# Kernel tuning notes

Measured on AMD Instinct MI355X. Metric: run time of the kernel, lower is better.

The kernel has to match this reference:

```python
import jax, jax.numpy as jnp
import numpy as np
from jax import lax

B, S, D, F = 2, 4096, 1024, 4096
LN_EPS = 1e-6

def _layer_norm(x, scale, bias):
    mu = jnp.mean(x, axis=-1, keepdims=True)
    var = jnp.mean(jnp.square(x - mu), axis=-1, keepdims=True)
    return (x - mu) * lax.rsqrt(var + LN_EPS) * scale + bias

def _gate_loop(q, k, v, a):
    # max-headed GateLoop: one head per channel, scalar complex state per channel
    # h_t = a_t * h_{t-1} + k_t * v_t ; y_t = q_t * h_t
    kv = (k * v).astype(jnp.complex64)
    def comb(e1, e2):
        a1, x1 = e1
        a2, x2 = e2
        return (a1 * a2, a2 * x1 + x2)
    _, h = lax.associative_scan(comb, (a, kv), axis=1)
    return q.astype(jnp.complex64) * h

def setup_inputs() -> dict:
    key = jax.random.key(0)
    ks = jax.random.split(key, 12)
    sd = 1.0 / np.sqrt(D)
    sf = 1.0 / np.sqrt(F)
    return {
        "x": jax.random.normal(ks[0], (B, S, D), jnp.float32),
        "Wq": jax.random.normal(ks[1], (D, D), jnp.float32) * sd,
        "Wk": jax.random.normal(ks[2], (D, D), jnp.float32) * sd,
        "Wv": jax.random.normal(ks[3], (D, D), jnp.float32) * sd,
        "Wa": jax.random.normal(ks[4], (D, 2 * D), jnp.float32) * sd,
        "Wg": jax.random.normal(ks[5], (D, D), jnp.float32) * sd,
        "Wo": jax.random.normal(ks[6], (D, D), jnp.float32) * sd,
        "ln1_scale": jnp.ones((D,), jnp.float32),
        "ln1_bias": jnp.zeros((D,), jnp.float32),
        "W1": jax.random.normal(ks[7], (D, F), jnp.float32) * sd,
        "b1": jax.random.normal(ks[8], (F,), jnp.float32) * 1e-6,
        "W2": jax.random.normal(ks[9], (F, D), jnp.float32) * sf,
        "b2": jax.random.normal(ks[10], (D,), jnp.float32) * 1e-6,
        "ln2_scale": jnp.ones((D,), jnp.float32),
        "ln2_bias": jnp.zeros((D,), jnp.float32),
    }

def reference(x, Wq, Wk, Wv, Wa, Wg, Wo, ln1_scale, ln1_bias, W1, b1, W2, b2, ln2_scale, ln2_bias):
    q = x @ Wq
    k = x @ Wk
    v = x @ Wv
    a = x @ Wa
    a_real, a_imag = jnp.split(a, 2, axis=-1)
    a_c = a_real + 1j * a_imag
    magnitude = jnp.abs(a_c)
    phase = jnp.angle(a_c)
    a_c = jax.nn.sigmoid(magnitude).astype(jnp.complex64) * jnp.exp(1j * phase)
    g = x.astype(jnp.complex64) @ Wg.astype(jnp.complex64)
    y = _gate_loop(q, k, v, a_c)
    y = y * (g * jax.nn.sigmoid(g))  # silu on complex g
    y = y @ Wo.astype(jnp.complex64)
    y = y.real
    # dropout deterministic (training=False)
    y = _layer_norm(y + x, ln1_scale, ln1_bias)
    h = jax.nn.gelu(y @ W1 + b1)
    out = h @ W2 + b2
    out = _layer_norm(out + y, ln2_scale, ln2_bias)
    return out
```

## Files before the change

### kernel.cpp

```cpp
#include <hip/hip_runtime.h>
#include <cstdint>

typedef unsigned short u16;
typedef unsigned int u32;

#define AS1 __attribute__((address_space(1)))
#define AS3 __attribute__((address_space(3)))

typedef _Float16 f16x8 __attribute__((ext_vector_type(8)));
typedef float f32x4 __attribute__((ext_vector_type(4)));

static constexpr int Bb = 2, Ss = 4096, Dd = 1024, Ff = 4096;
static constexpr int Mtok = Bb * Ss;
static constexpr int NCH = 128;
static constexpr int TCH = Ss / NCH;
static constexpr int PW = 6144;

__device__ __forceinline__ float h2f(u16 u) {
    union { u16 u; _Float16 h; } w; w.u = u; return (float)w.h;
}
__device__ __forceinline__ u16 f2h(float f) {
    union { _Float16 h; u16 u; } w; w.h = (_Float16)f; return w.u;
}

__device__ __forceinline__ void gload_lds16(const u16* g, u16* l) {
    __builtin_amdgcn_global_load_lds((const AS1 u32*)g, (AS3 u32*)l, 16, 0, 0);
}

__global__ __launch_bounds__(256) void cvt_f32_f16(const float* __restrict__ src,
                                                   u16* __restrict__ dst) {
    const long i = ((long)blockIdx.x * 256 + threadIdx.x) * 4;
    float4 f = *(const float4*)(src + i);
    ushort4 o;
    o.x = f2h(f.x); o.y = f2h(f.y); o.z = f2h(f.z); o.w = f2h(f.w);
    *(ushort4*)(dst + i) = o;
}

__global__ __launch_bounds__(1024) void transpose_f32_f16(const float* __restrict__ src,
                                                          u16* __restrict__ dst,
                                                          int K, int N) {
    __shared__ u16 t[32][33];
    const int tx = threadIdx.x, ty = threadIdx.y;
    const int n0 = blockIdx.x * 32, k0 = blockIdx.y * 32;
    t[ty][tx] = f2h(src[(long)(k0 + ty) * N + n0 + tx]);
    __syncthreads();
    dst[(long)(n0 + ty) * K + k0 + tx] = t[tx][ty];
}

template <int EPI>
__global__ __launch_bounds__(256, 2) void gemm_bt(const u16* __restrict__ A,
                                                  const u16* __restrict__ BT,
                                                  u16* __restrict__ C,
                                                  const float* __restrict__ bias,
                                                  int M, int N, int K,
                                                  int lda, int ldc) {
    __shared__ __align__(16) u16 sA[128 * 32];
    __shared__ __align__(16) u16 sB[128 * 32];
    const int tid = threadIdx.x;
    const int tm = blockIdx.y * 128;
    const int tn = blockIdx.x * 128;
    const int w = tid >> 6;
    const int lane = tid & 63;
    const int wm = (w >> 1) * 64;
    const int wn = (w & 1) * 64;
    const int q = lane >> 4;
    const int r16 = lane & 15;

    f32x4 acc[4][4];
#pragma unroll
    for (int i = 0; i < 4; i++)
#pragma unroll
        for (int j = 0; j < 4; j++) acc[i][j] = (f32x4){0.f, 0.f, 0.f, 0.f};

    const int s0 = tid, s1 = 256 + tid;
    const int row0 = s0 >> 2, kc0 = (s0 & 3) * 8;
    const int row1 = s1 >> 2, kc1 = (s1 & 3) * 8;
    const u16* Ar0 = A + (long)(tm + row0) * lda + kc0;
    const u16* Ar1 = A + (long)(tm + row1) * lda + kc1;
    const u16* Br0 = BT + (long)(tn + row0) * K + kc0;
    const u16* Br1 = BT + (long)(tn + row1) * K + kc1;

    const int kiters = K >> 5;
    for (int kt = 0; kt < kiters; ++kt) {
        const int ko = kt * 32;
        gload_lds16(Ar0 + ko, sA + s0 * 8);
        gload_lds16(Ar1 + ko, sA + s1 * 8);
        gload_lds16(Br0 + ko, sB + s0 * 8);
        gload_lds16(Br1 + ko, sB + s1 * 8);
        __syncthreads();
        f16x8 af[4], bfr[4];
#pragma unroll
        for (int mi = 0; mi < 4; mi++)
            af[mi] = *(const f16x8*)(sA + (wm + mi * 16 + r16) * 32 + q * 8);
#pragma unroll
        for (int ni = 0; ni < 4; ni++)
            bfr[ni] = *(const f16x8*)(sB + (wn + ni * 16 + r16) * 32 + q * 8);
#pragma unroll
        for (int mi = 0; mi < 4; mi++)
#pragma unroll
            for (int ni = 0; ni < 4; ni++)
                acc[mi][ni] = __builtin_amdgcn_mfma_f32_16x16x32_f16(
                    af[mi], bfr[ni], acc[mi][ni], 0, 0, 0);
        __syncthreads();
    }

#pragma unroll
    for (int mi = 0; mi < 4; mi++) {
#pragma unroll
        for (int ni = 0; ni < 4; ni++) {
            const int gcol = tn + wn + ni * 16 + r16;
            float bv = 0.f;
            if (EPI) bv = bias[gcol];
#pragma unroll
            for (int j = 0; j < 4; j++) {
                const int grow = tm + wm + mi * 16 + q * 4 + j;
                float v = acc[mi][ni][j];
                if (EPI) v += bv;
                if (EPI == 1) {
                    float t = tanhf(0.7978845608028654f * (v + 0.044715f * v * v * v));
                    v = 0.5f * v * (1.0f + t);
                }
                C[(long)grow * ldc + gcol] = f2h(v);
            }
        }
    }
}

__device__ __forceinline__ void a_transform(float ar, float ai, float& cr, float& ci) {
    float m = sqrtf(ar * ar + ai * ai);
    float sg = 1.f / (1.f + __expf(-m));
    float sc = sg / fmaxf(m, 1e-30f);
    cr = ar * sc;
    ci = ai * sc;
}

__global__ __launch_bounds__(1024) void scan1(const u16* __restrict__ pcat,
                                              float4* __restrict__ sum4) {
    const int b = blockIdx.y, c = blockIdx.x, d = threadIdx.x;
    float Arp = 1.f, Aip = 0.f, Xr = 0.f, Xi = 0.f;
    const long rowbase = (long)b * Ss + (long)c * TCH;
#pragma unroll 4
    for (int s = 0; s < TCH; ++s) {
        const long ro = (rowbase + s) * PW;
        float ar = h2f(pcat[ro + 3072 + d]);
        float ai = h2f(pcat[ro + 4096 + d]);
        float kk = h2f(pcat[ro + 1024 + d]);
        float vv = h2f(pcat[ro + 2048 + d]);
        float cr, ci;
        a_transform(ar, ai, cr, ci);
        float kv = kk * vv;
        float nXr = cr * Xr - ci * Xi + kv;
        float nXi = cr * Xi + ci * Xr;
        Xr = nXr; Xi = nXi;
        float nAr = cr * Arp - ci * Aip;
        float nAi = cr * Aip + ci * Arp;
        Arp = nAr; Aip = nAi;
    }
    sum4[((long)b * NCH + c) * 1024 + d] = make_float4(Arp, Aip, Xr, Xi);
}

__global__ __launch_bounds__(256) void scan2(const float4* __restrict__ sum4,
                                             float2* __restrict__ carry) {
    const int idx = blockIdx.x * 256 + threadIdx.x;
    const int b = idx >> 10, d = idx & 1023;
    float hr = 0.f, hi = 0.f;
    for (int cb = 0; cb < NCH / 8; ++cb) {
        float4 t[8];
#pragma unroll
        for (int j = 0; j < 8; j++)
            t[j] = sum4[((long)b * NCH + cb * 8 + j) * 1024 + d];
#pragma unroll
        for (int j = 0; j < 8; j++) {
            carry[((long)b * NCH + cb * 8 + j) * 1024 + d] = make_float2(hr, hi);
            float nr = t[j].x * hr - t[j].y * hi + t[j].z;
            float ni = t[j].x * hi + t[j].y * hr + t[j].w;
            hr = nr; hi = ni;
        }
    }
}

__global__ __launch_bounds__(1024) void scan3(u16* pcat,
                                              const float2* __restrict__ carry) {
    const int b = blockIdx.y, c = blockIdx.x, d = threadIdx.x;
    float2 h0 = carry[((long)b * NCH + c) * 1024 + d];
    float hr = h0.x, hi = h0.y;
    const long rowbase = (long)b * Ss + (long)c * TCH;
#pragma unroll 4
    for (int s = 0; s < TCH; ++s) {
        const long ro = (rowbase + s) * PW;
        float ar = h2f(pcat[ro + 3072 + d]);
        float ai = h2f(pcat[ro + 4096 + d]);
        float kk = h2f(pcat[ro + 1024 + d]);
        float vv = h2f(pcat[ro + 2048 + d]);
        float cr, ci;
        a_transform(ar, ai, cr, ci);
        float kv = kk * vv;
        float nhr = cr * hr - ci * hi + kv;
        float nhi = cr * hi + ci * hr;
        hr = nhr; hi = nhi;
        float gg = h2f(pcat[ro + 5120 + d]);
        float si = gg / (1.f + __expf(-gg));
        float yv = h2f(pcat[ro + d]) * hr * si;
        pcat[ro + d] = f2h(yv);
    }
}

template <int RESF32, int OUTF32>
__global__ __launch_bounds__(256) void ln_kernel(const u16* __restrict__ a, int sa,
                                                 const void* __restrict__ bres, int sres,
                                                 const float* __restrict__ scale,
                                                 const float* __restrict__ bias,
                                                 void* __restrict__ out, int sout) {
    const int row = blockIdx.x;
    const int tid = threadIdx.x;
    const long abase = (long)row * sa;
    const long rbase = (long)row * sres;
    const long obase = (long)row * sout;
    float v[4];
#pragma unroll
    for (int j = 0; j < 4; j++) {
        int d = tid * 4 + j;
        float rb = RESF32 ? ((const float*)bres)[rbase + d]
                          : h2f(((const u16*)bres)[rbase + d]);
        v[j] = h2f(a[abase + d]) + rb;
    }
    float s = v[0] + v[1] + v[2] + v[3];
    float s2 = v[0] * v[0] + v[1] * v[1] + v[2] * v[2] + v[3] * v[3];
#pragma unroll
    for (int off = 32; off; off >>= 1) {
        s += __shfl_down(s, off);
        s2 += __shfl_down(s2, off);
    }
    __shared__ float red[8];
    const int w = tid >> 6, lane = tid & 63;
    if (lane == 0) { red[w] = s; red[4 + w] = s2; }
    __syncthreads();
    if (tid == 0) {
        float ts = red[0] + red[1] + red[2] + red[3];
        float ts2 = red[4] + red[5] + red[6] + red[7];
        float mu = ts * (1.f / 1024.f);
        float var = ts2 * (1.f / 1024.f) - mu * mu;
        red[0] = mu;
        red[1] = rsqrtf(var + 1e-6f);
    }
    __syncthreads();
    const float mu = red[0], rs = red[1];
#pragma unroll
    for (int j = 0; j < 4; j++) {
        int d = tid * 4 + j;
        float y = (v[j] - mu) * rs * scale[d] + bias[d];
        if (OUTF32) ((float*)out)[obase + d] = y;
        else        ((u16*)out)[obase + d] = f2h(y);
    }
}

extern "C" void kernel_launch(void* const* d_in, const int* in_sizes, int n_in,
                              void* d_out, int out_size, void* d_ws, size_t ws_size,
                              hipStream_t stream) {
    const float* x    = (const float*)d_in[0];
    const float* Wq   = (const float*)d_in[1];
    const float* Wk   = (const float*)d_in[2];
    const float* Wv   = (const float*)d_in[3];
    const float* Wa   = (const float*)d_in[4];
    const float* Wg   = (const float*)d_in[5];
    const float* Wo   = (const float*)d_in[6];
    const float* ln1s = (const float*)d_in[7];
    const float* ln1b = (const float*)d_in[8];
    const float* W1   = (const float*)d_in[9];
    const float* b1   = (const float*)d_in[10];
    const float* W2   = (const float*)d_in[11];
    const float* b2   = (const float*)d_in[12];
    const float* ln2s = (const float*)d_in[13];
    const float* ln2b = (const float*)d_in[14];

    u16* ws    = (u16*)d_ws;
    u16* xb    = ws;
    u16* WTcat = xb + (8u << 20);
    u16* WTo   = WTcat + (6u << 20);
    u16* WT1   = WTo + (1u << 20);
    u16* WT2   = WT1 + (4u << 20);
    u16* pcat  = WT2 + (4u << 20);

    float4* sum4  = (float4*)WTcat;
    float2* carry = (float2*)(WTcat + (2u << 20));


    cvt_f32_f16<<<dim3(8192), dim3(256), 0, stream>>>(x, xb);

    const dim3 tb(32, 32);
    transpose_f32_f16<<<dim3(32, 32), tb, 0, stream>>>(Wq, WTcat, 1024, 1024);
    transpose_f32_f16<<<dim3(32, 32), tb, 0, stream>>>(Wk, WTcat + (1u << 20), 1024, 1024);
    transpose_f32_f16<<<dim3(32, 32), tb, 0, stream>>>(Wv, WTcat + (2u << 20), 1024, 1024);
    transpose_f32_f16<<<dim3(64, 32), tb, 0, stream>>>(Wa, WTcat + (3u << 20), 1024, 2048);
    transpose_f32_f16<<<dim3(32, 32), tb, 0, stream>>>(Wg, WTcat + (5u << 20), 1024, 1024);
    transpose_f32_f16<<<dim3(32, 32), tb, 0, stream>>>(Wo, WTo, 1024, 1024);
    transpose_f32_f16<<<dim3(128, 32), tb, 0, stream>>>(W1, WT1, 1024, 4096);
    transpose_f32_f16<<<dim3(32, 128), tb, 0, stream>>>(W2, WT2, 4096, 1024);

    const dim3 gblk(256);
    gemm_bt<0><<<dim3(48, 64), gblk, 0, stream>>>(xb, WTcat, pcat, nullptr,
                                                  Mtok, PW, 1024, 1024, PW);
    scan1<<<dim3(NCH, Bb), 1024, 0, stream>>>(pcat, sum4);
    scan2<<<dim3(8), 256, 0, stream>>>(sum4, carry);
    scan3<<<dim3(NCH, Bb), 1024, 0, stream>>>(pcat, carry);
    gemm_bt<0><<<dim3(8, 64), gblk, 0, stream>>>(pcat, WTo, pcat + 1024, nullptr,
                                                 Mtok, 1024, 1024, PW, PW);
    ln_kernel<1, 0><<<dim3(Mtok), gblk, 0, stream>>>(pcat + 1024, PW, x, 1024,
                                                     ln1s, ln1b, pcat, PW);
    gemm_bt<1><<<dim3(32, 64), gblk, 0, stream>>>(pcat, WT1, pcat + 2048, b1,
                                                  Mtok, Ff, 1024, PW, PW);
    gemm_bt<2><<<dim3(8, 64), gblk, 0, stream>>>(pcat + 2048, WT2, pcat + 1024, b2,
                                                 Mtok, 1024, Ff, PW, PW);
    ln_kernel<0, 1><<<dim3(Mtok), gblk, 0, stream>>>(pcat + 1024, PW, pcat, PW,
                                                     ln2s, ln2b, d_out, 1024);
}
```

Measured before the change: 607.1 us.

## Double GEMM K-tile to 64 and remap blocks per XCD for L2 locality

The GEMM kernel now stages 64-wide K slices in shared memory instead of 32, so each block has half as many sync barriers per unit of work and twice as many MFMAs between barriers. Block indices are also remapped so that consecutive blocks placed on the same XCD cover neighbouring N tiles, which should improve L2 reuse. In exchange each block uses twice the LDS (32 KB), and the 64-halfword row stride may cause more LDS bank conflicts. The remap assumes gridDim.x is a multiple of 8.

```diff
diff --git a/kernel.cpp b/kernel.cpp
--- a/kernel.cpp
+++ b/kernel.cpp
@@ -54,11 +54,20 @@
                                                   const float* __restrict__ bias,
                                                   int M, int N, int K,
                                                   int lda, int ldc) {
-    __shared__ __align__(16) u16 sA[128 * 32];
-    __shared__ __align__(16) u16 sB[128 * 32];
+    __shared__ __align__(16) u16 sA[128 * 64];
+    __shared__ __align__(16) u16 sB[128 * 64];
     const int tid = threadIdx.x;
-    const int tm = blockIdx.y * 128;
-    const int tn = blockIdx.x * 128;
+
+    const int nxt = gridDim.x;
+    const int id = blockIdx.x + nxt * blockIdx.y;
+    const int xcd = id & 7;
+    const int g = id >> 3;
+    const int xpg = nxt >> 3;
+    const int bx = xcd * xpg + (g % xpg);
+    const int by = g / xpg;
+
+    const int tm = by * 128;
+    const int tn = bx * 128;
     const int w = tid >> 6;
     const int lane = tid & 63;
     const int wm = (w >> 1) * 64;
@@ -72,35 +81,38 @@
 #pragma unroll
         for (int j = 0; j < 4; j++) acc[i][j] = (f32x4){0.f, 0.f, 0.f, 0.f};
 
-    const int s0 = tid, s1 = 256 + tid;
-    const int row0 = s0 >> 2, kc0 = (s0 & 3) * 8;
-    const int row1 = s1 >> 2, kc1 = (s1 & 3) * 8;
-    const u16* Ar0 = A + (long)(tm + row0) * lda + kc0;
-    const u16* Ar1 = A + (long)(tm + row1) * lda + kc1;
-    const u16* Br0 = BT + (long)(tn + row0) * K + kc0;
-    const u16* Br1 = BT + (long)(tn + row1) * K + kc1;
-
-    const int kiters = K >> 5;
+    const int srow = tid >> 3;
+    const int schk = (tid & 7) * 8;
+    const u16* Arow = A + (long)(tm + srow) * lda + schk;
+    const u16* Brow = BT + (long)(tn + srow) * K + schk;
+    const long astep = (long)32 * lda;
+    const long bstep = (long)32 * K;
+
+    const int kiters = K >> 6;
     for (int kt = 0; kt < kiters; ++kt) {
-        const int ko = kt * 32;
-        gload_lds16(Ar0 + ko, sA + s0 * 8);
-        gload_lds16(Ar1 + ko, sA + s1 * 8);
-        gload_lds16(Br0 + ko, sB + s0 * 8);
-        gload_lds16(Br1 + ko, sB + s1 * 8);
+        const int ko = kt * 64;
+#pragma unroll
+        for (int p = 0; p < 4; p++) {
+            gload_lds16(Arow + p * astep + ko, sA + (p * 256 + tid) * 8);
+            gload_lds16(Brow + p * bstep + ko, sB + (p * 256 + tid) * 8);
+        }
         __syncthreads();
-        f16x8 af[4], bfr[4];
-#pragma unroll
-        for (int mi = 0; mi < 4; mi++)
-            af[mi] = *(const f16x8*)(sA + (wm + mi * 16 + r16) * 32 + q * 8);
-#pragma unroll
-        for (int ni = 0; ni < 4; ni++)
-            bfr[ni] = *(const f16x8*)(sB + (wn + ni * 16 + r16) * 32 + q * 8);
-#pragma unroll
-        for (int mi = 0; mi < 4; mi++)
+#pragma unroll
+        for (int h = 0; h < 2; h++) {
+            f16x8 af[4], bfr[4];
+#pragma unroll
+            for (int mi = 0; mi < 4; mi++)
+                af[mi] = *(const f16x8*)(sA + (wm + mi * 16 + r16) * 64 + h * 32 + q * 8);
 #pragma unroll
             for (int ni = 0; ni < 4; ni++)
-                acc[mi][ni] = __builtin_amdgcn_mfma_f32_16x16x32_f16(
-                    af[mi], bfr[ni], acc[mi][ni], 0, 0, 0);
+                bfr[ni] = *(const f16x8*)(sB + (wn + ni * 16 + r16) * 64 + h * 32 + q * 8);
+#pragma unroll
+            for (int mi = 0; mi < 4; mi++)
+#pragma unroll
+                for (int ni = 0; ni < 4; ni++)
+                    acc[mi][ni] = __builtin_amdgcn_mfma_f32_16x16x32_f16(
+                        af[mi], bfr[ni], acc[mi][ni], 0, 0, 0);
+        }
         __syncthreads();
     }
 
```

Result: no change. 611.0 us (+0.6%).
